# Kernel optimization log

Measured on AMD Instinct MI355X. Metric: run time of the kernel, lower is better.

The kernel has to match this reference:

```python
import jax, jax.numpy as jnp
import numpy as np

N = 100000
E = 1600000
IN_FEATS = 256
HID = 128


def _graph_conv(x, W, b, src, dst, n_nodes):
    # DGL GraphConv with norm='both':
    #   out = D_in^{-1/2} * A * (D_out^{-1/2} * x @ W) + b
    ones = jnp.ones(src.shape[0], dtype=x.dtype)
    deg_out = jax.ops.segment_sum(ones, src, num_segments=n_nodes)
    deg_in = jax.ops.segment_sum(ones, dst, num_segments=n_nodes)
    norm_src = jnp.maximum(deg_out, 1.0) ** -0.5  # [N]
    norm_dst = jnp.maximum(deg_in, 1.0) ** -0.5   # [N]
    h = (x * norm_src[:, None]) @ W               # [N, HID]
    msg = h[src]                                  # [E, HID] gather
    agg = jax.ops.segment_sum(msg, dst, num_segments=n_nodes)  # [N, HID] scatter-add
    return agg * norm_dst[:, None] + b


def setup_inputs() -> dict:
    key = jax.random.key(0)
    ks = jax.random.split(key, 12)
    x = jax.random.normal(ks[0], (N, IN_FEATS), dtype=jnp.float32)
    src0 = jax.random.randint(ks[1], (E,), 0, N, dtype=jnp.int32)
    dst0 = jax.random.randint(ks[2], (E,), 0, N, dtype=jnp.int32)
    src1 = jax.random.randint(ks[3], (E,), 0, N, dtype=jnp.int32)
    dst1 = jax.random.randint(ks[4], (E,), 0, N, dtype=jnp.int32)
    s_e = 1.0 / np.sqrt(IN_FEATS)
    s_h = 1.0 / np.sqrt(HID)
    We = jax.random.uniform(ks[5], (IN_FEATS, HID), jnp.float32, -s_e, s_e)
    be = jax.random.uniform(ks[6], (HID,), jnp.float32, -s_e, s_e)
    W1 = jax.random.uniform(ks[7], (HID, HID), jnp.float32, -s_h, s_h)
    b1 = jnp.zeros((HID,), jnp.float32)
    W2 = jax.random.uniform(ks[8], (HID, HID), jnp.float32, -s_h, s_h)
    b2 = jnp.zeros((HID,), jnp.float32)
    return {"x": x, "We": We, "be": be, "W1": W1, "b1": b1, "W2": W2, "b2": b2,
            "src0": src0, "dst0": dst0, "src1": src1, "dst1": dst1}


def reference(x, We, be, W1, b1, W2, b2, src0, dst0, src1, dst1):
    n = x.shape[0]
    h = x @ We + be                                   # embed
    h = jax.nn.relu(_graph_conv(h, W1, b1, src0, dst0, n))
    h = jax.nn.relu(_graph_conv(h, W2, b2, src1, dst1, n))
    return h
```

## Files before the change

### kernel.cpp

```cpp
#include <hip/hip_runtime.h>

#define HID 128
#define NBUCK 512
#define BSHIFT 8
#define NB 512
#define M4 (4 * NBUCK * NB)
#define STAGE_CAP 8192

typedef __attribute__((ext_vector_type(8))) short bf16x8;
typedef __attribute__((ext_vector_type(4))) float f32x4;

__device__ __forceinline__ unsigned short f2bf(float f) {
    union { float f; unsigned u; } v; v.f = f;
    unsigned r = v.u + 0x7fff + ((v.u >> 16) & 1);
    return (unsigned short)(r >> 16);
}
__device__ __forceinline__ float bf2f(unsigned short b) {
    union { float f; unsigned u; } v; v.u = ((unsigned)b) << 16;
    return v.f;
}

__device__ __forceinline__ void gload_lds16(const void* g, void* l) {
    __builtin_amdgcn_global_load_lds(
        (const __attribute__((address_space(1))) void*)g,
        (__attribute__((address_space(3))) void*)l, 16, 0, 0);
}

__global__ __launch_bounds__(256) void bucket_count_all(
    const int* __restrict__ k0, const int* __restrict__ k1,
    const int* __restrict__ k2, const int* __restrict__ k3,
    int* __restrict__ counts, int E, int chunk) {
    __shared__ int h[4][NBUCK];
    int tid = threadIdx.x;
    #pragma unroll
    for (int j = 0; j < 8; ++j) ((int*)h)[tid + j * 256] = 0;
    __syncthreads();
    int base = blockIdx.x * chunk;
    int end = min(base + chunk, E);
    const int* keys[4] = {k0, k1, k2, k3};
    #pragma unroll
    for (int p = 0; p < 4; ++p) {
        const int* kp = keys[p];
        for (int i = base + tid; i < end; i += 256)
            atomicAdd(&h[p][kp[i] >> BSHIFT], 1);
    }
    __syncthreads();
    #pragma unroll
    for (int p = 0; p < 4; ++p) {
        counts[((p << 9) + tid) * NB + blockIdx.x] = h[p][tid];
        counts[((p << 9) + tid + 256) * NB + blockIdx.x] = h[p][tid + 256];
    }
}

__global__ __launch_bounds__(256) void scan_a(int* __restrict__ data, int* __restrict__ partials, int m) {
    __shared__ int sdata[256];
    int base = blockIdx.x * 1024;
    int tid = threadIdx.x;
    int v[4]; int s = 0;
    #pragma unroll
    for (int i = 0; i < 4; ++i) { int idx = base + tid * 4 + i; v[i] = (idx < m) ? data[idx] : 0; s += v[i]; }
    sdata[tid] = s; __syncthreads();
    for (int off = 1; off < 256; off <<= 1) {
        int t = (tid >= off) ? sdata[tid - off] : 0; __syncthreads();
        sdata[tid] += t; __syncthreads();
    }
    int excl = sdata[tid] - s;
    if (tid == 255) partials[blockIdx.x] = sdata[255];
    int run = excl;
    #pragma unroll
    for (int i = 0; i < 4; ++i) { int idx = base + tid * 4 + i; if (idx < m) data[idx] = run; run += v[i]; }
}

__global__ __launch_bounds__(1024) void scan_b(int* __restrict__ partials, int nb) {
    __shared__ int sdata[1024];
    int tid = threadIdx.x;
    int v = (tid < nb) ? partials[tid] : 0;
    sdata[tid] = v; __syncthreads();
    for (int off = 1; off < 1024; off <<= 1) {
        int t = (tid >= off) ? sdata[tid - off] : 0; __syncthreads();
        sdata[tid] += t; __syncthreads();
    }
    if (tid < nb) partials[tid] = sdata[tid] - v;
}

__global__ __launch_bounds__(256) void scan_c(int* __restrict__ data, const int* __restrict__ partials, int m) {
    int i = blockIdx.x * 256 + threadIdx.x;
    if (i < m) data[i] += partials[i >> 10];
}

__global__ __launch_bounds__(256) void bucket_scatter_all(
    const int* __restrict__ k0, const int* __restrict__ k1,
    const int* __restrict__ k2, const int* __restrict__ k3,
    const int* __restrict__ pay0, const int* __restrict__ pay1,
    const int* __restrict__ scanned, unsigned* __restrict__ bucketed,
    int E, int chunk) {
    __shared__ unsigned cur[4][NBUCK];
    int tid = threadIdx.x;
    int blk = blockIdx.x;
    #pragma unroll
    for (int p = 0; p < 4; ++p) {
        cur[p][tid]       = (unsigned)scanned[((p << 9) + tid) * NB + blk];
        cur[p][tid + 256] = (unsigned)scanned[((p << 9) + tid + 256) * NB + blk];
    }
    __syncthreads();
    int base = blk * chunk;
    int end = min(base + chunk, E);
    const int* keys[4] = {k0, k1, k2, k3};
    const int* pays[4] = {pay0, pay1, nullptr, nullptr};
    #pragma unroll
    for (int p = 0; p < 4; ++p) {
        const int* kp = keys[p];
        const int* pp = pays[p];
        for (int i = base + tid; i < end; i += 256) {
            int k = kp[i];
            int b = k >> BSHIFT;
            unsigned pay = pp ? (unsigned)pp[i] : 0u;
            unsigned pos = atomicAdd(&cur[p][b], 1u);
            bucketed[pos] = ((unsigned)(k & 255) << 17) | pay;
        }
    }
}

__global__ __launch_bounds__(256) void bucket_finalize(
    unsigned* __restrict__ bucketed, const int* __restrict__ scanned,
    int* __restrict__ rowptr0, int* __restrict__ rowptr1,
    int* __restrict__ dout0, int* __restrict__ dout1, int n, int E) {
    __shared__ unsigned stage[STAGE_CAP];
    __shared__ int cnt[256];
    __shared__ int sd[256];
    __shared__ int excl[256];
    __shared__ int cur[256];
    int tid = threadIdx.x;
    int g = blockIdx.x;
    int p = g >> 9;
    int b = g & 511;
    int start = scanned[g * NB];
    int end = (g == 4 * NBUCK - 1) ? 4 * E : scanned[(g + 1) * NB];
    if (end - start > STAGE_CAP) end = start + STAGE_CAP;
    int len = end - start;
    int node0 = b << BSHIFT;

    cnt[tid] = 0;
    __syncthreads();
    if (p < 2) {
        for (int i = tid; i < len; i += 256) {
            unsigned v = bucketed[start + i];
            stage[i] = v;
            atomicAdd(&cnt[v >> 17], 1);
        }
    } else {
        for (int i = tid; i < len; i += 256)
            atomicAdd(&cnt[bucketed[start + i] >> 17], 1);
    }
    __syncthreads();

    if (p >= 2) {
        int* dout = (p == 2) ? dout0 : dout1;
        int node = node0 + tid;
        if (node < n) dout[node] = cnt[tid];
        return;
    }

    int v = cnt[tid];
    sd[tid] = v;
    __syncthreads();
    for (int off = 1; off < 256; off <<= 1) {
        int t = (tid >= off) ? sd[tid - off] : 0; __syncthreads();
        sd[tid] += t; __syncthreads();
    }
    excl[tid] = sd[tid] - v;
    cur[tid] = 0;
    __syncthreads();

    int startLocal = start - p * E;
    int* rp = (p == 0) ? rowptr0 : rowptr1;
    int node = node0 + tid;
    if (node < n) rp[node] = startLocal + excl[tid];
    if (b == NBUCK - 1 && tid == 0) rp[n] = E;

    int* csr = (int*)bucketed + p * E;
    for (int i = tid; i < len; i += 256) {
        unsigned w = stage[i];
        int nl = (int)(w >> 17);
        int pos = startLocal + excl[nl] + atomicAdd(&cur[nl], 1);
        csr[pos] = (int)(w & 0x1FFFFu);
    }
}

__device__ __forceinline__ size_t bswz_idx(int k, int col) {
    int s = k >> 5, lh = (k >> 3) & 3, j = k & 7;
    int c = col >> 4, lc = col & 15;
    return ((((size_t)s * 8 + c) * 64 + (lh * 16 + lc)) * 8 + j);
}

__global__ __launch_bounds__(256) void weight_fuse(
    const float* __restrict__ We, const float* __restrict__ be,
    const float* __restrict__ W1,
    unsigned short* __restrict__ B1h, unsigned short* __restrict__ B1l,
    float* __restrict__ cv) {
    __shared__ float w1[128][128];
    int tid = threadIdx.x;
    #pragma unroll
    for (int it = 0; it < 16; ++it) {
        int s = tid + it * 256;
        int r = s >> 5, c4 = (s & 31) << 2;
        *(float4*)&w1[r][c4] = *(const float4*)&W1[r * 128 + c4];
    }
    __syncthreads();
    int j = tid & 127;
    int half = tid >> 7;
    if (blockIdx.x == 128) {
        if (half) return;
        float sum = 0.f;
        for (int k = 0; k < 128; ++k) sum += be[k] * w1[k][j];
        cv[j] = sum;
        return;
    }
    int i = blockIdx.x * 2 + half;
    const float* arow = &We[i * 128];
    float sum = 0.f;
    for (int k = 0; k < 128; ++k) sum += arow[k] * w1[k][j];
    unsigned short h = f2bf(sum);
    unsigned short l = f2bf(sum - bf2f(h));
    size_t o = bswz_idx(i, j);
    B1h[o] = h; B1l[o] = l;
}

__global__ __launch_bounds__(256) void swizzle_split(
    const float* __restrict__ W, unsigned short* __restrict__ Bh,
    unsigned short* __restrict__ Bl, int K) {
    int idx = blockIdx.x * 256 + threadIdx.x;
    if (idx >= K * 128) return;
    int k = idx >> 7, col = idx & 127;
    float v = W[idx];
    unsigned short h = f2bf(v);
    unsigned short l = f2bf(v - bf2f(h));
    size_t o = bswz_idx(k, col);
    Bh[o] = h; Bl[o] = l;
}

template <int K, bool AFP32>
__global__ __launch_bounds__(256) void gemm_lds(
    const void* __restrict__ X_,
    const unsigned short* __restrict__ Bh, const unsigned short* __restrict__ Bl,
    const float* __restrict__ cvec, const int* __restrict__ degs,
    unsigned short* __restrict__ T, int n) {
    constexpr int NS = K / 32;
    __shared__ __align__(16) char smem[2 * 16384];
    const int tid = threadIdx.x;
    const int wave = tid >> 6;
    const int lane = tid & 63;
    const int lr = lane & 15;
    const int lk = lane >> 4;
    const int row0 = blockIdx.x * 64 + wave * 16;
    const int grow = row0 + lr;
    const bool vr = grow < n;

    f32x4 acc[8];
    #pragma unroll
    for (int c = 0; c < 8; ++c) acc[c] = (f32x4)0.f;

    auto stage_slab = [&](int s, char* dst) {
        #pragma unroll
        for (int it = 0; it < 4; ++it) {
            int u = tid + it * 256;
            int f = u >> 6;
            int c = f >> 1, plane = f & 1;
            const unsigned short* srcArr = plane ? Bl : Bh;
            const char* g = (const char*)srcArr +
                ((size_t)(s * 512 + c * 64 + (u & 63)) * 16);
            gload_lds16(g, dst + u * 16);
        }
    };

    stage_slab(0, smem);

    const float* pxf = AFP32 ? (const float*)X_ + (size_t)grow * K + lk * 8 : nullptr;
    const unsigned short* pxb = AFP32 ? nullptr : (const unsigned short*)X_ + (size_t)grow * K + lk * 8;
    float4 a0 = make_float4(0.f, 0.f, 0.f, 0.f), a1 = a0;
    bf16x8 ab = (bf16x8)0;
    if (AFP32) {
        if (vr) { a0 = *(const float4*)pxf; a1 = *(const float4*)(pxf + 4); }
    } else {
        if (vr) ab = *(const bf16x8*)pxb;
    }

    #pragma unroll
    for (int s = 0; s < NS; ++s) {
        __syncthreads();
        if (s + 1 < NS) stage_slab(s + 1, smem + ((s + 1) & 1) * 16384);

        float4 n0 = make_float4(0.f, 0.f, 0.f, 0.f), n1 = n0;
        bf16x8 nb = (bf16x8)0;
        if (s + 1 < NS && vr) {
            if (AFP32) {
                n0 = *(const float4*)(pxf + (s + 1) * 32);
                n1 = *(const float4*)(pxf + (s + 1) * 32 + 4);
            } else {
                nb = *(const bf16x8*)(pxb + (s + 1) * 32);
            }
        }

        bf16x8 ah, al;
        if (AFP32) {
            float av[8] = {a0.x, a0.y, a0.z, a0.w, a1.x, a1.y, a1.z, a1.w};
            #pragma unroll
            for (int j = 0; j < 8; ++j) {
                unsigned short h = f2bf(av[j]);
                ah[j] = (short)h;
                al[j] = (short)f2bf(av[j] - bf2f(h));
            }
        } else {
            ah = ab;
        }

        const char* base = smem + (s & 1) * 16384 + lane * 16;
        #pragma unroll
        for (int c = 0; c < 8; ++c) {
            bf16x8 bh = *(const bf16x8*)(base + (c * 2) * 1024);
            bf16x8 bl = *(const bf16x8*)(base + (c * 2 + 1) * 1024);
            acc[c] = __builtin_amdgcn_mfma_f32_16x16x32_bf16(ah, bh, acc[c], 0, 0, 0);
            acc[c] = __builtin_amdgcn_mfma_f32_16x16x32_bf16(ah, bl, acc[c], 0, 0, 0);
            if (AFP32)
                acc[c] = __builtin_amdgcn_mfma_f32_16x16x32_bf16(al, bh, acc[c], 0, 0, 0);
        }
        a0 = n0; a1 = n1; ab = nb;
    }

    #pragma unroll
    for (int r = 0; r < 4; ++r) {
        int orow = row0 + lk * 4 + r;
        if (orow >= n) continue;
        float norm = rsqrtf(fmaxf((float)degs[orow], 1.0f));
        #pragma unroll
        for (int c = 0; c < 8; ++c) {
            float v = acc[c][r];
            if (cvec) v += cvec[c * 16 + lr];
            T[(size_t)orow * 128 + c * 16 + lr] = f2bf(v * norm);
        }
    }
}

template <bool OUT_BF16>
__global__ __launch_bounds__(256) void aggregate(
    const unsigned short* __restrict__ T, const int* __restrict__ rowptr,
    const int* __restrict__ csr, const float* __restrict__ bias,
    void* __restrict__ out_, int n) {
    const int wave = threadIdx.x >> 6;
    const int lane = threadIdx.x & 63;
    const int half = lane >> 5;
    const int l32 = lane & 31;
    const int node = blockIdx.x * 4 + wave;
    if (node >= n) return;
    const int beg = rowptr[node], end = rowptr[node + 1];
    float a0 = 0.f, a1 = 0.f, a2 = 0.f, a3 = 0.f;
    int e = beg;
    for (; e + 15 < end; e += 16) {
        int sidx[8];
        #pragma unroll
        for (int j = 0; j < 8; ++j) sidx[j] = csr[e + j * 2 + half];
        #pragma unroll
        for (int j = 0; j < 8; ++j) {
            uint2 u = *(const uint2*)&T[(size_t)sidx[j] * 128 + l32 * 4];
            a0 += __uint_as_float(u.x << 16);
            a1 += __uint_as_float(u.x & 0xffff0000u);
            a2 += __uint_as_float(u.y << 16);
            a3 += __uint_as_float(u.y & 0xffff0000u);
        }
    }
    for (; e + 1 < end; e += 2) {
        int sidx = csr[e + half];
        uint2 u = *(const uint2*)&T[(size_t)sidx * 128 + l32 * 4];
        a0 += __uint_as_float(u.x << 16);
        a1 += __uint_as_float(u.x & 0xffff0000u);
        a2 += __uint_as_float(u.y << 16);
        a3 += __uint_as_float(u.y & 0xffff0000u);
    }
    if (e < end && half == 0) {
        int sidx = csr[e];
        uint2 u = *(const uint2*)&T[(size_t)sidx * 128 + l32 * 4];
        a0 += __uint_as_float(u.x << 16);
        a1 += __uint_as_float(u.x & 0xffff0000u);
        a2 += __uint_as_float(u.y << 16);
        a3 += __uint_as_float(u.y & 0xffff0000u);
    }
    a0 += __shfl_xor(a0, 32);
    a1 += __shfl_xor(a1, 32);
    a2 += __shfl_xor(a2, 32);
    a3 += __shfl_xor(a3, 32);
    if (half == 0) {
        float norm = rsqrtf(fmaxf((float)(end - beg), 1.0f));
        float4 bv = *(const float4*)&bias[l32 * 4];
        float o0 = fmaxf(a0 * norm + bv.x, 0.f);
        float o1 = fmaxf(a1 * norm + bv.y, 0.f);
        float o2 = fmaxf(a2 * norm + bv.z, 0.f);
        float o3 = fmaxf(a3 * norm + bv.w, 0.f);
        if (OUT_BF16) {
            unsigned w0 = (unsigned)f2bf(o0) | ((unsigned)f2bf(o1) << 16);
            unsigned w1 = (unsigned)f2bf(o2) | ((unsigned)f2bf(o3) << 16);
            uint2* dst = (uint2*)((unsigned short*)out_ + (size_t)node * 128 + l32 * 4);
            *dst = make_uint2(w0, w1);
        } else {
            float4* dst = (float4*)((float*)out_ + (size_t)node * 128 + l32 * 4);
            *dst = make_float4(o0, o1, o2, o3);
        }
    }
}

extern "C" void kernel_launch(void* const* d_in, const int* in_sizes, int n_in,
                              void* d_out, int out_size, void* d_ws, size_t ws_size,
                              hipStream_t stream) {
    const float* x   = (const float*)d_in[0];
    const float* We  = (const float*)d_in[1];
    const float* be  = (const float*)d_in[2];
    const float* W1  = (const float*)d_in[3];
    const float* b1  = (const float*)d_in[4];
    const float* W2  = (const float*)d_in[5];
    const float* b2  = (const float*)d_in[6];
    const int* src0  = (const int*)d_in[7];
    const int* dst0  = (const int*)d_in[8];
    const int* src1  = (const int*)d_in[9];
    const int* dst1  = (const int*)d_in[10];
    float* out = (float*)d_out;

    const int n = in_sizes[0] / 256;
    const int E = in_sizes[7];
    const int chunk = (E + NB - 1) / NB;

    char* p = (char*)d_ws;
    auto carve = [&](size_t bytes) -> void* {
        void* r = (void*)p;
        p += (bytes + 511) & ~(size_t)511;
        return r;
    };
    unsigned short* t        = (unsigned short*)carve((size_t)n * HID * 2);
    unsigned short* h1       = (unsigned short*)carve((size_t)n * HID * 2);
    unsigned*       bucketed = (unsigned*)carve((size_t)4 * E * 4);
    int*            counts   = (int*)carve((size_t)M4 * 4);
    int*            partials = (int*)carve(1024 * 4);
    int*            rowptr0  = (int*)carve(((size_t)n + 1) * 4);
    int*            rowptr1  = (int*)carve(((size_t)n + 1) * 4);
    int*            dout0    = (int*)carve((size_t)n * 4);
    int*            dout1    = (int*)carve((size_t)n * 4);
    unsigned short* B1h      = (unsigned short*)carve(256 * HID * 2);
    unsigned short* B1l      = (unsigned short*)carve(256 * HID * 2);
    unsigned short* B2h      = (unsigned short*)carve(128 * HID * 2);
    unsigned short* B2l      = (unsigned short*)carve(128 * HID * 2);
    float*          cv       = (float*)carve(HID * 4);

    int* csr0 = (int*)bucketed;
    int* csr1 = (int*)bucketed + E;

    const int gGemm  = (n + 63) / 64;
    const int gAggN  = (n + 3) / 4;
    const int gScanA = (M4 + 1023) / 1024;
    const int gScanC = (M4 + 255) / 256;

    bucket_count_all<<<NB, 256, 0, stream>>>(dst0, dst1, src0, src1, counts, E, chunk);
    scan_a<<<gScanA, 256, 0, stream>>>(counts, partials, M4);
    scan_b<<<1, 1024, 0, stream>>>(partials, gScanA);
    scan_c<<<gScanC, 256, 0, stream>>>(counts, partials, M4);
    bucket_scatter_all<<<NB, 256, 0, stream>>>(dst0, dst1, src0, src1, src0, src1,
                                               counts, bucketed, E, chunk);
    bucket_finalize<<<4 * NBUCK, 256, 0, stream>>>(bucketed, counts, rowptr0, rowptr1, dout0, dout1, n, E);

    weight_fuse<<<129, 256, 0, stream>>>(We, be, W1, B1h, B1l, cv);
    swizzle_split<<<(128 * 128 + 255) / 256, 256, 0, stream>>>(W2, B2h, B2l, 128);

    gemm_lds<256, true><<<gGemm, 256, 0, stream>>>((const void*)x, B1h, B1l, cv, dout0, t, n);
    aggregate<true><<<gAggN, 256, 0, stream>>>(t, rowptr0, csr0, b1, (void*)h1, n);
    gemm_lds<128, false><<<gGemm, 256, 0, stream>>>((const void*)h1, B2h, B2l, nullptr, dout1, t, n);
    aggregate<false><<<gAggN, 256, 0, stream>>>(t, rowptr1, csr1, b2, (void*)out, n);
}
```

Measured before the change: 326.9 us.

## Double rows per wave and stage four K-slabs of B per LDS phase

Each wave now computes two 16-row MFMA tiles instead of one, so every B fragment read from LDS is reused twice, and the block covers 128 rows. B staging changes from double-buffered 32-wide slabs to 64 KB phases holding four slabs, with barriers only between phases. This cuts LDS traffic and barrier count per output but uses 64 KB of LDS and more accumulator registers, which lowers occupancy and drops the overlap of B loads with compute.

```diff
diff --git a/kernel.cpp b/kernel.cpp
--- a/kernel.cpp
+++ b/kernel.cpp
@@ -246,97 +246,130 @@
     const float* __restrict__ cvec, const int* __restrict__ degs,
     unsigned short* __restrict__ T, int n) {
     constexpr int NS = K / 32;
-    __shared__ __align__(16) char smem[2 * 16384];
+    constexpr int NPH = K / 128;
+    __shared__ __align__(16) char smem[65536];
     const int tid = threadIdx.x;
     const int wave = tid >> 6;
     const int lane = tid & 63;
     const int lr = lane & 15;
     const int lk = lane >> 4;
-    const int row0 = blockIdx.x * 64 + wave * 16;
-    const int grow = row0 + lr;
-    const bool vr = grow < n;
-
-    f32x4 acc[8];
-    #pragma unroll
-    for (int c = 0; c < 8; ++c) acc[c] = (f32x4)0.f;
-
-    auto stage_slab = [&](int s, char* dst) {
+    const int row0 = blockIdx.x * 128 + wave * 32;
+    const int r0 = row0 + lr;
+    const int r1 = row0 + 16 + lr;
+    const bool v0 = r0 < n, v1 = r1 < n;
+
+    f32x4 acc[2][8];
+    #pragma unroll
+    for (int t = 0; t < 2; ++t)
         #pragma unroll
-        for (int it = 0; it < 4; ++it) {
+        for (int c = 0; c < 8; ++c) acc[t][c] = (f32x4)0.f;
+
+    auto stage_slab = [&](int ph) {
+        #pragma unroll
+        for (int it = 0; it < 16; ++it) {
             int u = tid + it * 256;
             int f = u >> 6;
-            int c = f >> 1, plane = f & 1;
+            int plane = f & 1;
+            int c = (f >> 1) & 7;
+            int sl = f >> 4;
             const unsigned short* srcArr = plane ? Bl : Bh;
             const char* g = (const char*)srcArr +
-                ((size_t)(s * 512 + c * 64 + (u & 63)) * 16);
-            gload_lds16(g, dst + u * 16);
+                ((size_t)((ph * 4 + sl) * 512 + c * 64 + (u & 63)) * 16);
+            gload_lds16(g, smem + u * 16);
         }
     };
 
-    stage_slab(0, smem);
-
-    const float* pxf = AFP32 ? (const float*)X_ + (size_t)grow * K + lk * 8 : nullptr;
-    const unsigned short* pxb = AFP32 ? nullptr : (const unsigned short*)X_ + (size_t)grow * K + lk * 8;
-    float4 a0 = make_float4(0.f, 0.f, 0.f, 0.f), a1 = a0;
-    bf16x8 ab = (bf16x8)0;
-    if (AFP32) {
-        if (vr) { a0 = *(const float4*)pxf; a1 = *(const float4*)(pxf + 4); }
-    } else {
-        if (vr) ab = *(const bf16x8*)pxb;
-    }
-
-    #pragma unroll
-    for (int s = 0; s < NS; ++s) {
-        __syncthreads();
-        if (s + 1 < NS) stage_slab(s + 1, smem + ((s + 1) & 1) * 16384);
-
-        float4 n0 = make_float4(0.f, 0.f, 0.f, 0.f), n1 = n0;
-        bf16x8 nb = (bf16x8)0;
-        if (s + 1 < NS && vr) {
+    const float* pxf0 = (const float*)X_ + (size_t)r0 * K + lk * 8;
+    const float* pxf1 = (const float*)X_ + (size_t)r1 * K + lk * 8;
+    const unsigned short* pxb0 = (const unsigned short*)X_ + (size_t)r0 * K + lk * 8;
+    const unsigned short* pxb1 = (const unsigned short*)X_ + (size_t)r1 * K + lk * 8;
+
+    auto loadA = [&](int s, float4 f[2][2], bf16x8 b[2]) {
+        if (AFP32) {
+            f[0][0] = make_float4(0.f, 0.f, 0.f, 0.f); f[0][1] = f[0][0];
+            f[1][0] = f[0][0]; f[1][1] = f[0][0];
+            if (v0) { f[0][0] = *(const float4*)(pxf0 + s * 32); f[0][1] = *(const float4*)(pxf0 + s * 32 + 4); }
+            if (v1) { f[1][0] = *(const float4*)(pxf1 + s * 32); f[1][1] = *(const float4*)(pxf1 + s * 32 + 4); }
+        } else {
+            b[0] = (bf16x8)0; b[1] = (bf16x8)0;
+            if (v0) b[0] = *(const bf16x8*)(pxb0 + s * 32);
+            if (v1) b[1] = *(const bf16x8*)(pxb1 + s * 32);
+        }
+    };
+
+    float4 af[2][2], nf[2][2];
+    bf16x8 abv[2], nbv[2];
+
+    stage_slab(0);
+    loadA(0, af, abv);
+    __syncthreads();
+
+    #pragma unroll
+    for (int ph = 0; ph < NPH; ++ph) {
+        #pragma unroll
+        for (int sl = 0; sl < 4; ++sl) {
+            const int s = ph * 4 + sl;
+            if (s + 1 < NS) loadA(s + 1, nf, nbv);
+
+            bf16x8 ah[2], al[2];
             if (AFP32) {
-                n0 = *(const float4*)(pxf + (s + 1) * 32);
-                n1 = *(const float4*)(pxf + (s + 1) * 32 + 4);
+                #pragma unroll
+                for (int t = 0; t < 2; ++t) {
+                    float av[8] = {af[t][0].x, af[t][0].y, af[t][0].z, af[t][0].w,
+                                   af[t][1].x, af[t][1].y, af[t][1].z, af[t][1].w};
+                    #pragma unroll
+                    for (int j = 0; j < 8; ++j) {
+                        unsigned short h = f2bf(av[j]);
+                        ah[t][j] = (short)h;
+                        al[t][j] = (short)f2bf(av[j] - bf2f(h));
+                    }
+                }
             } else {
-                nb = *(const bf16x8*)(pxb + (s + 1) * 32);
+                ah[0] = abv[0]; ah[1] = abv[1];
+                al[0] = (bf16x8)0; al[1] = (bf16x8)0;
             }
-        }
-
-        bf16x8 ah, al;
-        if (AFP32) {
-            float av[8] = {a0.x, a0.y, a0.z, a0.w, a1.x, a1.y, a1.z, a1.w};
+
+            const char* base = smem + sl * 16384 + lane * 16;
             #pragma unroll
-            for (int j = 0; j < 8; ++j) {
-                unsigned short h = f2bf(av[j]);
-                ah[j] = (short)h;
-                al[j] = (short)f2bf(av[j] - bf2f(h));
+            for (int c = 0; c < 8; ++c) {
+                bf16x8 bh = *(const bf16x8*)(base + (c * 2) * 1024);
+                bf16x8 bl = *(const bf16x8*)(base + (c * 2 + 1) * 1024);
+                #pragma unroll
+                for (int t = 0; t < 2; ++t) {
+                    acc[t][c] = __builtin_amdgcn_mfma_f32_16x16x32_bf16(ah[t], bh, acc[t][c], 0, 0, 0);
+                    acc[t][c] = __builtin_amdgcn_mfma_f32_16x16x32_bf16(ah[t], bl, acc[t][c], 0, 0, 0);
+                    if (AFP32)
+                        acc[t][c] = __builtin_amdgcn_mfma_f32_16x16x32_bf16(al[t], bh, acc[t][c], 0, 0, 0);
+                }
             }
-        } else {
-            ah = ab;
-        }
-
-        const char* base = smem + (s & 1) * 16384 + lane * 16;
+
+            if (AFP32) {
+                #pragma unroll
+                for (int t = 0; t < 2; ++t) { af[t][0] = nf[t][0]; af[t][1] = nf[t][1]; }
+            } else {
+                abv[0] = nbv[0]; abv[1] = nbv[1];
+            }
+        }
+        if (ph + 1 < NPH) {
+            __syncthreads();
+            stage_slab(ph + 1);
+            __syncthreads();
+        }
+    }
+
+    #pragma unroll
+    for (int t = 0; t < 2; ++t) {
         #pragma unroll
-        for (int c = 0; c < 8; ++c) {
-            bf16x8 bh = *(const bf16x8*)(base + (c * 2) * 1024);
-            bf16x8 bl = *(const bf16x8*)(base + (c * 2 + 1) * 1024);
-            acc[c] = __builtin_amdgcn_mfma_f32_16x16x32_bf16(ah, bh, acc[c], 0, 0, 0);
-            acc[c] = __builtin_amdgcn_mfma_f32_16x16x32_bf16(ah, bl, acc[c], 0, 0, 0);
-            if (AFP32)
-                acc[c] = __builtin_amdgcn_mfma_f32_16x16x32_bf16(al, bh, acc[c], 0, 0, 0);
-        }
-        a0 = n0; a1 = n1; ab = nb;
-    }
-
-    #pragma unroll
-    for (int r = 0; r < 4; ++r) {
-        int orow = row0 + lk * 4 + r;
-        if (orow >= n) continue;
-        float norm = rsqrtf(fmaxf((float)degs[orow], 1.0f));
-        #pragma unroll
-        for (int c = 0; c < 8; ++c) {
-            float v = acc[c][r];
-            if (cvec) v += cvec[c * 16 + lr];
-            T[(size_t)orow * 128 + c * 16 + lr] = f2bf(v * norm);
+        for (int r = 0; r < 4; ++r) {
+            int orow = row0 + t * 16 + lk * 4 + r;
+            if (orow >= n) continue;
+            float norm = rsqrtf(fmaxf((float)degs[orow], 1.0f));
+            #pragma unroll
+            for (int c = 0; c < 8; ++c) {
+                float v = acc[t][c][r];
+                if (cvec) v += cvec[c * 16 + lr];
+                T[(size_t)orow * 128 + c * 16 + lr] = f2bf(v * norm);
+            }
         }
     }
 }
@@ -451,7 +484,7 @@
     int* csr0 = (int*)bucketed;
     int* csr1 = (int*)bucketed + E;
 
-    const int gGemm  = (n + 63) / 64;
+    const int gGemm  = (n + 127) / 128;
     const int gAggN  = (n + 3) / 4;
     const int gScanA = (M4 + 1023) / 1024;
     const int gScanC = (M4 + 255) / 256;
```

Result: slower. 343.3 us (+5.0%).
